# Kernel tuning notes

Hardware: AMD Instinct MI355X
Metric: run time of the kernel (lower is better)

The kernel has to match this reference:

```python
import jax, jax.numpy as jnp
import numpy as np

B, S, D = 2, 2048, 1024
H, E = 16, 64          # n_heads, head_dim
DFF = 4096             # intermediate
R_ATTN, R_OUT, R_FF = 32, 512, 512
LN_EPS = 1e-5
SCALE = 1.0 / np.sqrt(E)


def setup_inputs() -> dict:
    key = jax.random.key(0)
    ks = jax.random.split(key, 24)
    s = 0.02
    inp = {
        "hidden_states": jax.random.normal(ks[0], (B, S, D), jnp.float32),
        "ln1_w": jnp.ones((D,), jnp.float32),
        "ln1_b": jnp.zeros((D,), jnp.float32),
        "q_U": jax.random.normal(ks[1], (H, E, R_ATTN), jnp.float32) * s,
        "q_V": jax.random.normal(ks[2], (H, R_ATTN, D), jnp.float32) * s,
        "q_bias": jax.random.normal(ks[3], (H, E), jnp.float32) * s,
        "k_U": jax.random.normal(ks[4], (H, E, R_ATTN), jnp.float32) * s,
        "k_V": jax.random.normal(ks[5], (H, R_ATTN, D), jnp.float32) * s,
        "k_bias": jax.random.normal(ks[6], (H, E), jnp.float32) * s,
        "v_U": jax.random.normal(ks[7], (H, E, R_ATTN), jnp.float32) * s,
        "v_V": jax.random.normal(ks[8], (H, R_ATTN, D), jnp.float32) * s,
        "v_bias": jax.random.normal(ks[9], (H, E), jnp.float32) * s,
        "out_U": jax.random.normal(ks[10], (D, R_OUT), jnp.float32) * s,
        "out_V": jax.random.normal(ks[11], (R_OUT, D), jnp.float32) * s,
        "out_bias": jnp.zeros((D,), jnp.float32),
        "ln2_w": jnp.ones((D,), jnp.float32),
        "ln2_b": jnp.zeros((D,), jnp.float32),
        "fc1_U": jax.random.normal(ks[12], (DFF, R_FF), jnp.float32) * s,
        "fc1_V": jax.random.normal(ks[13], (R_FF, D), jnp.float32) * s,
        "fc1_bias": jnp.zeros((DFF,), jnp.float32),
        "fc2_U": jax.random.normal(ks[14], (D, R_FF), jnp.float32) * s,
        "fc2_V": jax.random.normal(ks[15], (R_FF, DFF), jnp.float32) * s,
        "fc2_bias": jnp.zeros((D,), jnp.float32),
    }
    return inp


def _layernorm(x, w, b):
    mu = jnp.mean(x, axis=-1, keepdims=True)
    var = jnp.mean(jnp.square(x - mu), axis=-1, keepdims=True)
    return (x - mu) * jax.lax.rsqrt(var + LN_EPS) * w + b


def _per_head_svd(x, U, V, bias):
    # x: [b,s,d]; V: [h,r,d]; U: [h,e,r]; bias: [h,e] -> [b,h,s,e]
    t = jnp.einsum("bsd,hrd->bhsr", x, V)
    return jnp.einsum("bhsr,her->bhse", t, U) + bias[None, :, None, :]


def reference(hidden_states, ln1_w, ln1_b, q_U, q_V, q_bias, k_U, k_V, k_bias,
              v_U, v_V, v_bias, out_U, out_V, out_bias, ln2_w, ln2_b,
              fc1_U, fc1_V, fc1_bias, fc2_U, fc2_V, fc2_bias):
    b, s, d = hidden_states.shape
    normed = _layernorm(hidden_states, ln1_w, ln1_b)

    q = _per_head_svd(normed, q_U, q_V, q_bias)  # [b,h,s,e]
    k = _per_head_svd(normed, k_U, k_V, k_bias)
    v = _per_head_svd(normed, v_U, v_V, v_bias)

    scores = jnp.einsum("bhqe,bhke->bhqk", q, k) * SCALE
    causal = jnp.tril(jnp.ones((s, s), dtype=bool))
    scores = jnp.where(causal, scores, -jnp.inf)
    probs = jax.nn.softmax(scores, axis=-1)
    attn = jnp.einsum("bhqk,bhke->bhqe", probs, v)
    attn = attn.transpose(0, 2, 1, 3).reshape(b, s, d)  # [b,s,d]

    attn = jnp.einsum("bsr,dr->bsd", jnp.einsum("bsd,rd->bsr", attn, out_V), out_U) + out_bias
    hidden_states = hidden_states + attn

    normed = _layernorm(hidden_states, ln2_w, ln2_b)
    ff = jnp.einsum("bsr,fr->bsf", jnp.einsum("bsd,rd->bsr", normed, fc1_V), fc1_U) + fc1_bias
    ff = jax.nn.gelu(ff, approximate=False)  # exact erf gelu as in torch F.gelu
    ff = jnp.einsum("bsr,dr->bsd", jnp.einsum("bsf,rf->bsr", ff, fc2_V), fc2_U) + fc2_bias
    hidden_states = hidden_states + ff
    return (hidden_states,)
```

## Files before the change

kernel.cpp:

```cpp
#include <hip/hip_runtime.h>
#include <hip/hip_bf16.h>
#include <math.h>

#define Bc 2
#define Sc 2048
#define Dc 1024
#define Hc 16
#define Ec 64
#define DFFc 4096
#define SCALEc 0.125f
#define SCLOG2E 0.18033688f
#define LN_EPSc 1e-5f
#define BH_STRIDE 131072

typedef short bf16x8 __attribute__((ext_vector_type(8)));
typedef unsigned short u16x4 __attribute__((ext_vector_type(4)));
typedef unsigned short u16x8 __attribute__((ext_vector_type(8)));
typedef float f32x4 __attribute__((ext_vector_type(4)));
typedef float f32x16 __attribute__((ext_vector_type(16)));
typedef unsigned int u32x4 __attribute__((ext_vector_type(4)));
#define MFMA16(a, b, c) __builtin_amdgcn_mfma_f32_16x16x32_bf16(a, b, c, 0, 0, 0)
#define MFMA32(a, b, c) __builtin_amdgcn_mfma_f32_32x32x16_bf16(a, b, c, 0, 0, 0)
#define GLDS16(g, l)                                                            \
  __builtin_amdgcn_global_load_lds((const __attribute__((address_space(1))) void*)(g), \
                                   (__attribute__((address_space(3))) void*)(l), 16, 0, 0)

static __device__ __forceinline__ unsigned short f2bf(float x) {
  unsigned u = __float_as_uint(x);
  unsigned r = (u + 0x7FFFu + ((u >> 16) & 1u)) >> 16;
  return (unsigned short)r;
}
static __device__ __forceinline__ unsigned cvtpk(float lo, float hi) {
  unsigned r;
  asm("v_cvt_pk_bf16_f32 %0, %1, %2" : "=v"(r) : "v"(lo), "v"(hi));
  return r;
}

__global__ __launch_bounds__(256) void convert9(
    const float* __restrict__ s0, const float* __restrict__ s1, const float* __restrict__ s2,
    const float* __restrict__ s3, const float* __restrict__ s4, const float* __restrict__ s5,
    const float* __restrict__ s6, const float* __restrict__ s7, const float* __restrict__ s8,
    unsigned short* __restrict__ wsu) {
  int i = (blockIdx.x * 256 + threadIdx.x) * 4;
  const float* s;
  int off;
  if (i < 3145728) {
    int seg = i >> 19;
    off = i & 524287;
    s = (seg == 0) ? s0 : (seg == 1) ? s1 : (seg == 2) ? s2
        : (seg == 3) ? s3 : (seg == 4) ? s4 : s5;
  } else if (i < 5242880) { s = s6; off = i - 3145728; }
  else if (i < 7340032)   { s = s7; off = i - 5242880; }
  else if (i < 7864320)   { s = s8; off = i - 7340032; }
  else return;
  float4 v = *(const float4*)(s + off);
  u16x4 o = {f2bf(v.x), f2bf(v.y), f2bf(v.z), f2bf(v.w)};
  *(u16x4*)(wsu + i) = o;
}

__global__ __launch_bounds__(256) void ln_bf16(const float* __restrict__ x,
                                               const float* __restrict__ w,
                                               const float* __restrict__ b,
                                               unsigned short* __restrict__ out) {
  __shared__ float sm[8];
  int row = blockIdx.x;
  int tid = threadIdx.x;
  const float* xr = x + (size_t)row * Dc;
  float v[4];
  float sum = 0.f;
#pragma unroll
  for (int i = 0; i < 4; ++i) { v[i] = xr[tid + i * 256]; sum += v[i]; }
#pragma unroll
  for (int off = 32; off > 0; off >>= 1) sum += __shfl_down(sum, off, 64);
  if ((tid & 63) == 0) sm[tid >> 6] = sum;
  __syncthreads();
  float mean = (sm[0] + sm[1] + sm[2] + sm[3]) * (1.f / Dc);
  float var = 0.f;
#pragma unroll
  for (int i = 0; i < 4; ++i) { float d0 = v[i] - mean; var += d0 * d0; }
#pragma unroll
  for (int off = 32; off > 0; off >>= 1) var += __shfl_down(var, off, 64);
  if ((tid & 63) == 0) sm[4 + (tid >> 6)] = var;
  __syncthreads();
  float rstd = rsqrtf((sm[4] + sm[5] + sm[6] + sm[7]) * (1.f / Dc) + LN_EPSc);
  unsigned short* orow = out + (size_t)row * Dc;
#pragma unroll
  for (int i = 0; i < 4; ++i) {
    int c = tid + i * 256;
    orow[c] = f2bf((v[i] - mean) * rstd * w[c] + b[c]);
  }
}

template <int BM, int BN>
__global__ __launch_bounds__(256) void gemm_bf16(const unsigned short* __restrict__ A,
                                                 const unsigned short* __restrict__ W,
                                                 float* __restrict__ Cf,
                                                 unsigned short* __restrict__ Cb,
                                                 const float* __restrict__ bias,
                                                 const float* __restrict__ res,
                                                 int M, int N, int K, int gelu) {
  constexpr int BK = 64;
  constexpr int MT = BM / 32;
  constexpr int NT = BN / 32;
  __shared__ unsigned short As[2][BM * BK];
  __shared__ unsigned short Bs[2][BN * BK];
  int tid = threadIdx.x;
  int lane = tid & 63;
  int wid = tid >> 6;
  int cl = lane & 15, grp = lane >> 4;
  int wr = wid >> 1, wc = wid & 1;
  const unsigned short* Ab = A + (size_t)(blockIdx.y * BM) * K;
  const unsigned short* Wb = W + (size_t)(blockIdx.x * BN) * K;
  f32x4 acc[MT][NT];
  f32x4 z4 = {0.f, 0.f, 0.f, 0.f};
#pragma unroll
  for (int i = 0; i < MT; ++i)
#pragma unroll
    for (int j = 0; j < NT; ++j) acc[i][j] = z4;
  int r0 = tid >> 3;
  int c0 = (tid & 7) * 8;

#define STAGE(buf, k0)                                                         \
  {                                                                            \
    _Pragma("unroll") for (int l = 0; l < BM / 32; ++l) {                      \
      int row = r0 + l * 32;                                                   \
      int sc = c0 ^ ((row & 7) * 8);                                           \
      GLDS16(Ab + (size_t)row * K + (k0) + sc, &As[buf][(tid + l * 256) * 8]); \
    }                                                                          \
    _Pragma("unroll") for (int l = 0; l < BN / 32; ++l) {                      \
      int row = r0 + l * 32;                                                   \
      int sc = c0 ^ ((row & 7) * 8);                                           \
      GLDS16(Wb + (size_t)row * K + (k0) + sc, &Bs[buf][(tid + l * 256) * 8]); \
    }                                                                          \
  }

  int nt = K / BK;
  STAGE(0, 0)
  __syncthreads();
  for (int t = 0; t < nt; ++t) {
    int cur = t & 1;
    if (t + 1 < nt) STAGE(cur ^ 1, (t + 1) * BK)
#pragma unroll
    for (int kk = 0; kk < 2; ++kk) {
      bf16x8 af[MT], bfr[NT];
#pragma unroll
      for (int i = 0; i < MT; ++i) {
        int row = wr * (BM / 2) + i * 16 + cl;
        af[i] = *(const bf16x8*)&As[cur][row * BK + ((kk * 32 + grp * 8) ^ ((row & 7) * 8))];
      }
#pragma unroll
      for (int j = 0; j < NT; ++j) {
        int row = wc * (BN / 2) + j * 16 + cl;
        bfr[j] = *(const bf16x8*)&Bs[cur][row * BK + ((kk * 32 + grp * 8) ^ ((row & 7) * 8))];
      }
#pragma unroll
      for (int i = 0; i < MT; ++i)
#pragma unroll
        for (int j = 0; j < NT; ++j) acc[i][j] = MFMA16(af[i], bfr[j], acc[i][j]);
    }
    __syncthreads();
  }
#undef STAGE

#pragma unroll
  for (int i = 0; i < MT; ++i) {
    int row = blockIdx.y * BM + wr * (BM / 2) + i * 16 + grp * 4;
#pragma unroll
    for (int j = 0; j < NT; ++j) {
      int col = blockIdx.x * BN + wc * (BN / 2) + j * 16 + cl;
      float bv = bias ? bias[col] : 0.f;
#pragma unroll
      for (int r = 0; r < 4; ++r) {
        float v = acc[i][j][r] + bv;
        if (gelu) v = 0.5f * v * (1.f + erff(v * 0.70710678118f));
        if (res) v += res[(size_t)(row + r) * N + col];
        if (Cb) Cb[(size_t)(row + r) * N + col] = f2bf(v);
        else Cf[(size_t)(row + r) * N + col] = v;
      }
    }
  }
}

__global__ __launch_bounds__(256) void expand_all(const float* __restrict__ t,
                                                  const float* __restrict__ qU,
                                                  const float* __restrict__ kU,
                                                  const float* __restrict__ vU,
                                                  const float* __restrict__ qB,
                                                  const float* __restrict__ kB,
                                                  const float* __restrict__ vB,
                                                  unsigned short* __restrict__ qO,
                                                  unsigned short* __restrict__ kO,
                                                  unsigned short* __restrict__ vO) {
  __shared__ float Us[64][33];
  __shared__ float Ts[32][33];
  int blk = blockIdx.x;
  int kind = blk >> 11;
  int inner = blk & 2047;
  int sb = inner & 63;
  int h = (inner >> 6) & 15;
  int b = inner >> 10;
  int bh = b * Hc + h;
  int tid = threadIdx.x;
  const float* U = (kind == 0) ? qU : (kind == 1) ? kU : vU;
  const float* bias = (kind == 0) ? qB : (kind == 1) ? kB : vB;
  int toff = kind * 512;
  for (int i = tid; i < 64 * 32; i += 256) Us[i >> 5][i & 31] = U[h * 2048 + i];
  for (int i = tid; i < 32 * 32; i += 256) {
    int sr = i >> 5, r = i & 31;
    Ts[sr][r] = t[(size_t)(b * Sc + sb * 32 + sr) * 1536 + toff + h * 32 + r];
  }
  __syncthreads();
  if (kind < 2) {
    unsigned short* out = (kind == 0) ? qO : kO;
    float prescale = (kind == 0) ? SCLOG2E : 1.0f;
    int s = tid >> 3;
    int ec = tid & 7;
    float acc[8];
#pragma unroll
    for (int j = 0; j < 8; ++j) acc[j] = bias[h * 64 + ec * 8 + j];
    for (int r = 0; r < 32; ++r) {
      float tv = Ts[s][r];
#pragma unroll
      for (int j = 0; j < 8; ++j) acc[j] += tv * Us[ec * 8 + j][r];
    }
    u16x8 v8;
#pragma unroll
    for (int j = 0; j < 8; ++j) v8[j] = f2bf(acc[j] * prescale);
    int es = ec >> 1, hi = ec & 1;
    int lane = s + hi * 32;
    *(u16x8*)(out + (size_t)bh * BH_STRIDE + (size_t)(((sb * 4 + es) * 64 + lane)) * 8) = v8;
  } else {
    int e = tid & 63;
    int sg = tid >> 6;
    float bv = bias[h * 64 + e];
    u16x8 v8;
#pragma unroll
    for (int si = 0; si < 8; ++si) {
      int sr = sg * 8 + si;
      float acc = bv;
#pragma unroll
      for (int r = 0; r < 32; ++r) acc += Ts[sr][r] * Us[e][r];
      v8[si] = f2bf(acc);
    }
    int eo = e >> 5, ll = e & 31;
    int h2 = sg >> 1, hi = sg & 1;
    int ix = eo * 2 + h2;
    int lane = ll + hi * 32;
    *(u16x8*)(vO + (size_t)bh * BH_STRIDE + (size_t)(((sb * 4 + ix) * 64 + lane)) * 8) = v8;
  }
}

__global__ __launch_bounds__(256) void attn_mfma(const unsigned short* __restrict__ qf_,
                                                 const unsigned short* __restrict__ kf_,
                                                 const unsigned short* __restrict__ vf_,
                                                 unsigned short* __restrict__ out) {
  __shared__ float MS[2][34][64];
  int tid = threadIdx.x;
  int wid = tid >> 6;
  int lane = tid & 63;
  int ll = lane & 31;
  int hi = lane >> 5;
  int blk = blockIdx.x;
  int qt = 63 - (blk >> 5);
  int bh = blk & 31;
  int b = bh >> 4, h = bh & 15;
  const unsigned short* qb = qf_ + (size_t)bh * BH_STRIDE;
  const unsigned short* kb = kf_ + (size_t)bh * BH_STRIDE;
  const unsigned short* vb = vf_ + (size_t)bh * BH_STRIDE;
  int q0 = qt * 32;
  int nt = qt + 1;
  int full = nt - 1;
  int fs = wid * full / 4;
  int fe = (wid + 1) * full / 4;

  bf16x8 qf[4];
#pragma unroll
  for (int es = 0; es < 4; ++es)
    qf[es] = *(const bf16x8*)(qb + (size_t)((qt * 4 + es) * 64 + lane) * 8);

  f32x16 accO[2] = {};
  float m = -1e30f, l = 0.f;

  int t = fs;
  for (; t + 1 < fe; t += 2) {
    bf16x8 ka[4], kb2[4];
#pragma unroll
    for (int es = 0; es < 4; ++es) {
      ka[es] = *(const bf16x8*)(kb + (size_t)((t * 4 + es) * 64 + lane) * 8);
      kb2[es] = *(const bf16x8*)(kb + (size_t)(((t + 1) * 4 + es) * 64 + lane) * 8);
    }
    f32x16 cA = {}, cB = {};
    __builtin_amdgcn_s_setprio(1);
    cA = MFMA32(ka[0], qf[0], cA);
    cA = MFMA32(ka[1], qf[1], cA);
    cA = MFMA32(ka[2], qf[2], cA);
    cA = MFMA32(ka[3], qf[3], cA);
    cB = MFMA32(kb2[0], qf[0], cB);
    cB = MFMA32(kb2[1], qf[1], cB);
    cB = MFMA32(kb2[2], qf[2], cB);
    cB = MFMA32(kb2[3], qf[3], cB);
    __builtin_amdgcn_s_setprio(0);
    float s[32];
#pragma unroll
    for (int r = 0; r < 16; ++r) { s[r] = cA[r]; s[16 + r] = cB[r]; }
    float mx[16];
#pragma unroll
    for (int r = 0; r < 16; ++r) mx[r] = fmaxf(s[r], s[16 + r]);
#pragma unroll
    for (int st = 8; st > 0; st >>= 1)
#pragma unroll
      for (int r = 0; r < 8; ++r)
        if (r < st) mx[r] = fmaxf(mx[r], mx[r + st]);
    float tmax = fmaxf(mx[0], __shfl_xor(mx[0], 32, 64));
    if (!__all(tmax <= m)) {
      float mn = fmaxf(m, tmax);
      float corr = exp2f(m - mn);
      m = mn;
      l *= corr;
#pragma unroll
      for (int r = 0; r < 16; ++r) { accO[0][r] *= corr; accO[1][r] *= corr; }
    }
#pragma unroll
    for (int r = 0; r < 32; ++r) s[r] = exp2f(s[r] - m);
#pragma unroll
    for (int r = 0; r < 16; ++r) mx[r] = s[r] + s[16 + r];
#pragma unroll
    for (int st = 8; st > 0; st >>= 1)
#pragma unroll
      for (int r = 0; r < 8; ++r)
        if (r < st) mx[r] += mx[r + st];
    l += mx[0];
    bf16x8 va[4], vb2[4];
#pragma unroll
    for (int ix = 0; ix < 4; ++ix) {
      va[ix] = *(const bf16x8*)(vb + (size_t)((t * 4 + ix) * 64 + lane) * 8);
      vb2[ix] = *(const bf16x8*)(vb + (size_t)(((t + 1) * 4 + ix) * 64 + lane) * 8);
    }
    unsigned wA0 = cvtpk(s[0], s[1]), wA1 = cvtpk(s[2], s[3]);
    unsigned wA2 = cvtpk(s[4], s[5]), wA3 = cvtpk(s[6], s[7]);
    unsigned wA4 = cvtpk(s[8], s[9]), wA5 = cvtpk(s[10], s[11]);
    unsigned wA6 = cvtpk(s[12], s[13]), wA7 = cvtpk(s[14], s[15]);
    unsigned wB0 = cvtpk(s[16], s[17]), wB1 = cvtpk(s[18], s[19]);
    unsigned wB2 = cvtpk(s[20], s[21]), wB3 = cvtpk(s[22], s[23]);
    unsigned wB4 = cvtpk(s[24], s[25]), wB5 = cvtpk(s[26], s[27]);
    unsigned wB6 = cvtpk(s[28], s[29]), wB7 = cvtpk(s[30], s[31]);
    asm("v_permlane32_swap_b32 %0, %1" : "+v"(wA0), "+v"(wA2));
    asm("v_permlane32_swap_b32 %0, %1" : "+v"(wA1), "+v"(wA3));
    asm("v_permlane32_swap_b32 %0, %1" : "+v"(wA4), "+v"(wA6));
    asm("v_permlane32_swap_b32 %0, %1" : "+v"(wA5), "+v"(wA7));
    asm("v_permlane32_swap_b32 %0, %1" : "+v"(wB0), "+v"(wB2));
    asm("v_permlane32_swap_b32 %0, %1" : "+v"(wB1), "+v"(wB3));
    asm("v_permlane32_swap_b32 %0, %1" : "+v"(wB4), "+v"(wB6));
    asm("v_permlane32_swap_b32 %0, %1" : "+v"(wB5), "+v"(wB7));
    u32x4 pA0 = {wA0, wA1, wA2, wA3}, pA1 = {wA4, wA5, wA6, wA7};
    u32x4 pB0 = {wB0, wB1, wB2, wB3}, pB1 = {wB4, wB5, wB6, wB7};
    bf16x8 bA0 = __builtin_bit_cast(bf16x8, pA0), bA1 = __builtin_bit_cast(bf16x8, pA1);
    bf16x8 bB0 = __builtin_bit_cast(bf16x8, pB0), bB1 = __builtin_bit_cast(bf16x8, pB1);
    __builtin_amdgcn_s_setprio(1);
    accO[0] = MFMA32(va[0], bA0, accO[0]);
    accO[0] = MFMA32(va[1], bA1, accO[0]);
    accO[0] = MFMA32(vb2[0], bB0, accO[0]);
    accO[0] = MFMA32(vb2[1], bB1, accO[0]);
    accO[1] = MFMA32(va[2], bA0, accO[1]);
    accO[1] = MFMA32(va[3], bA1, accO[1]);
    accO[1] = MFMA32(vb2[2], bB0, accO[1]);
    accO[1] = MFMA32(vb2[3], bB1, accO[1]);
    __builtin_amdgcn_s_setprio(0);
  }

#define ATT_ONE(T, MASKED)                                                          \
  {                                                                                 \
    bf16x8 kf1[4];                                                                  \
    _Pragma("unroll") for (int es = 0; es < 4; ++es)                                \
      kf1[es] = *(const bf16x8*)(kb + (size_t)(((T) * 4 + es) * 64 + lane) * 8);    \
    f32x16 c = {};                                                                  \
    __builtin_amdgcn_s_setprio(1);                                                  \
    c = MFMA32(kf1[0], qf[0], c);                                                   \
    c = MFMA32(kf1[1], qf[1], c);                                                   \
    c = MFMA32(kf1[2], qf[2], c);                                                   \
    c = MFMA32(kf1[3], qf[3], c);                                                   \
    __builtin_amdgcn_s_setprio(0);                                                  \
    float s1[16];                                                                   \
    _Pragma("unroll") for (int r = 0; r < 16; ++r) {                                \
      s1[r] = c[r];                                                                 \
      if (MASKED) {                                                                 \
        int keyloc = (r & 3) + 8 * (r >> 2) + 4 * hi;                               \
        if (keyloc > ll) s1[r] = -1e30f;                                            \
      }                                                                             \
    }                                                                               \
    float u0 = fmaxf(fmaxf(fmaxf(s1[0], s1[1]), fmaxf(s1[2], s1[3])),               \
                     fmaxf(fmaxf(s1[4], s1[5]), fmaxf(s1[6], s1[7])));              \
    float u1 = fmaxf(fmaxf(fmaxf(s1[8], s1[9]), fmaxf(s1[10], s1[11])),             \
                     fmaxf(fmaxf(s1[12], s1[13]), fmaxf(s1[14], s1[15])));          \
    float tmax = fmaxf(u0, u1);                                                     \
    tmax = fmaxf(tmax, __shfl_xor(tmax, 32, 64));                                   \
    if (!__all(tmax <= m)) {                                                        \
      float mn = fmaxf(m, tmax);                                                    \
      float corr = exp2f(m - mn);                                                   \
      m = mn;                                                                       \
      l *= corr;                                                                    \
      _Pragma("unroll") for (int r = 0; r < 16; ++r) {                              \
        accO[0][r] *= corr; accO[1][r] *= corr;                                     \
      }                                                                             \
    }                                                                               \
    float lp = 0.f;                                                                 \
    _Pragma("unroll") for (int r = 0; r < 16; ++r) { s1[r] = exp2f(s1[r] - m); lp += s1[r]; } \
    l += lp;                                                                        \
    bf16x8 vf1[4];                                                                  \
    _Pragma("unroll") for (int ix = 0; ix < 4; ++ix)                                \
      vf1[ix] = *(const bf16x8*)(vb + (size_t)(((T) * 4 + ix) * 64 + lane) * 8);    \
    unsigned w0 = cvtpk(s1[0], s1[1]), w1 = cvtpk(s1[2], s1[3]);                    \
    unsigned w2 = cvtpk(s1[4], s1[5]), w3 = cvtpk(s1[6], s1[7]);                    \
    unsigned w4 = cvtpk(s1[8], s1[9]), w5 = cvtpk(s1[10], s1[11]);                  \
    unsigned w6 = cvtpk(s1[12], s1[13]), w7 = cvtpk(s1[14], s1[15]);                \
    asm("v_permlane32_swap_b32 %0, %1" : "+v"(w0), "+v"(w2));                       \
    asm("v_permlane32_swap_b32 %0, %1" : "+v"(w1), "+v"(w3));                       \
    asm("v_permlane32_swap_b32 %0, %1" : "+v"(w4), "+v"(w6));                       \
    asm("v_permlane32_swap_b32 %0, %1" : "+v"(w5), "+v"(w7));                       \
    u32x4 pw0 = {w0, w1, w2, w3};                                                   \
    u32x4 pw1 = {w4, w5, w6, w7};                                                   \
    bf16x8 pb0 = __builtin_bit_cast(bf16x8, pw0);                                   \
    bf16x8 pb1 = __builtin_bit_cast(bf16x8, pw1);                                   \
    __builtin_amdgcn_s_setprio(1);                                                  \
    accO[0] = MFMA32(vf1[0], pb0, accO[0]);                                         \
    accO[0] = MFMA32(vf1[1], pb1, accO[0]);                                         \
    accO[1] = MFMA32(vf1[2], pb0, accO[1]);                                         \
    accO[1] = MFMA32(vf1[3], pb1, accO[1]);                                         \
    __builtin_amdgcn_s_setprio(0);                                                  \
  }

  if (t < fe) ATT_ONE(t, false)
  if (wid == 3) ATT_ONE(full, true)
#undef ATT_ONE

  auto publish = [&](int slot) {
#pragma unroll
    for (int r = 0; r < 16; ++r) {
      MS[slot][r][lane] = accO[0][r];
      MS[slot][16 + r][lane] = accO[1][r];
    }
    MS[slot][32][lane] = m;
    MS[slot][33][lane] = l;
  };
  auto merge = [&](int slot) {
    float mw = MS[slot][32][lane];
    float lw = MS[slot][33][lane];
    float ms = fmaxf(m, mw);
    float sc = exp2f(m - ms);
    float sw = exp2f(mw - ms);
    m = ms;
    l = l * sc + lw * sw;
#pragma unroll
    for (int r = 0; r < 16; ++r) {
      accO[0][r] = accO[0][r] * sc + MS[slot][r][lane] * sw;
      accO[1][r] = accO[1][r] * sc + MS[slot][16 + r][lane] * sw;
    }
  };
  if (wid == 1) publish(0);
  if (wid == 3) publish(1);
  __syncthreads();
  if (wid == 0) merge(0);
  if (wid == 2) merge(1);
  __syncthreads();
  if (wid == 2) publish(0);
  __syncthreads();
  if (wid == 0) {
    merge(0);
    float ltot = l + __shfl_xor(l, 32, 64);
    float inv = 1.f / ltot;
    unsigned short* orow = out + (size_t)(b * Sc + q0 + ll) * Dc + h * Ec;
#pragma unroll
    for (int eo = 0; eo < 2; ++eo)
#pragma unroll
      for (int r = 0; r < 16; ++r) {
        int e = eo * 32 + (r & 3) + 8 * (r >> 2) + 4 * hi;
        orow[e] = f2bf(accO[eo][r] * inv);
      }
  }
}

extern "C" void kernel_launch(void* const* d_in, const int* in_sizes, int n_in,
                              void* d_out, int out_size, void* d_ws, size_t ws_size,
                              hipStream_t stream) {
  const float* hidden = (const float*)d_in[0];
  const float* ln1_w = (const float*)d_in[1];
  const float* ln1_b = (const float*)d_in[2];
  const float* q_U = (const float*)d_in[3];
  const float* q_V = (const float*)d_in[4];
  const float* q_bias = (const float*)d_in[5];
  const float* k_U = (const float*)d_in[6];
  const float* k_V = (const float*)d_in[7];
  const float* k_bias = (const float*)d_in[8];
  const float* v_U = (const float*)d_in[9];
  const float* v_V = (const float*)d_in[10];
  const float* v_bias = (const float*)d_in[11];
  const float* out_U = (const float*)d_in[12];
  const float* out_V = (const float*)d_in[13];
  const float* out_bias = (const float*)d_in[14];
  const float* ln2_w = (const float*)d_in[15];
  const float* ln2_b = (const float*)d_in[16];
  const float* fc1_U = (const float*)d_in[17];
  const float* fc1_V = (const float*)d_in[18];
  const float* fc1_bias = (const float*)d_in[19];
  const float* fc2_U = (const float*)d_in[20];
  const float* fc2_V = (const float*)d_in[21];
  const float* fc2_bias = (const float*)d_in[22];
  float* out = (float*)d_out;
  float* ws = (float*)d_ws;
  unsigned short* wsu = (unsigned short*)d_ws;

  unsigned short* wQKV = wsu;
  unsigned short* wOUTV = wsu + 1572864;
  unsigned short* wOUTU = wsu + 2097152;
  unsigned short* wFC1V = wsu + 2621440;
  unsigned short* wFC1U = wsu + 3145728;
  unsigned short* wFC2V = wsu + 5242880;
  unsigned short* wFC2U = wsu + 7340032;

  float* h1 = ws + 4194304;
  unsigned short* attn_out = (unsigned short*)(ws + 6291456);
  unsigned short* normed = (unsigned short*)(ws + 8388608);
  float* rb = ws + 10485760;
  unsigned short* rbB = (unsigned short*)(ws + 10485760);
  unsigned short* ff = (unsigned short*)(ws + 11534336);
  unsigned short* qbuf = (unsigned short*)(ws + 16777216);
  unsigned short* kbuf = (unsigned short*)(ws + 18874368);
  unsigned short* rbG = (unsigned short*)(ws + 19922944);
  unsigned short* vtbuf = (unsigned short*)(ws + 20971520);

  const int M = Bc * Sc;
  dim3 blk(256);

  convert9<<<7680, blk, 0, stream>>>(q_V, k_V, v_V, out_V, out_U, fc1_V, fc1_U, fc2_V, fc2_U, wsu);

  ln_bf16<<<M, blk, 0, stream>>>(hidden, ln1_w, ln1_b, normed);

  gemm_bf16<64, 64><<<dim3(24, 64), blk, 0, stream>>>(normed, wQKV, rb, nullptr, nullptr, nullptr,
                                                      M, 1536, Dc, 0);
  expand_all<<<6144, blk, 0, stream>>>(rb, q_U, k_U, v_U, q_bias, k_bias, v_bias,
                                       qbuf, kbuf, vtbuf);

  attn_mfma<<<2048, blk, 0, stream>>>(qbuf, kbuf, vtbuf, attn_out);

  gemm_bf16<64, 64><<<dim3(8, 64), blk, 0, stream>>>(attn_out, wOUTV, nullptr, rbB, nullptr, nullptr,
                                                     M, 512, Dc, 0);
  gemm_bf16<64, 64><<<dim3(16, 64), blk, 0, stream>>>(rbB, wOUTU, h1, nullptr, out_bias, hidden,
                                                      M, Dc, 512, 0);

  ln_bf16<<<M, blk, 0, stream>>>(h1, ln2_w, ln2_b, normed);
  gemm_bf16<64, 64><<<dim3(8, 64), blk, 0, stream>>>(normed, wFC1V, nullptr, rbB, nullptr, nullptr,
                                                     M, 512, Dc, 0);
  gemm_bf16<128, 64><<<dim3(64, 32), blk, 0, stream>>>(rbB, wFC1U, nullptr, ff, fc1_bias, nullptr,
                                                       M, DFFc, 512, 1);
  gemm_bf16<64, 64><<<dim3(8, 64), blk, 0, stream>>>(ff, wFC2V, nullptr, rbG, nullptr, nullptr,
                                                     M, 512, DFFc, 0);
  gemm_bf16<64, 64><<<dim3(16, 64), blk, 0, stream>>>(rbG, wFC2U, out, nullptr, fc2_bias, h1,
                                                      M, Dc, 512, 0);
}
```

Before: 281.4 us.

## Restructure attention to share LDS-staged K/V tiles across four query waves

The attention kernel changes from one 32-query tile per block (split-K across four waves with an LDS merge) to a 128-query tile per block where each wave owns 32 queries. K/V tiles of 64 keys are staged into double-buffered LDS with async global-to-LDS loads and shared by all four waves, which removes the cross-wave softmax merge and cuts redundant global K/V reads. The grid shrinks from 2048 to 512 blocks with a heavy/light ordering for causal balance. In exchange there is a barrier per tile, waves idle on tiles past their diagonal, and fewer blocks give less parallelism.

```diff
diff --git a/kernel.cpp b/kernel.cpp
--- a/kernel.cpp
+++ b/kernel.cpp
@@ -254,229 +254,156 @@
                                                  const unsigned short* __restrict__ kf_,
                                                  const unsigned short* __restrict__ vf_,
                                                  unsigned short* __restrict__ out) {
-  __shared__ float MS[2][34][64];
+  __shared__ unsigned short Ks[2][4096];
+  __shared__ unsigned short Vs[2][4096];
   int tid = threadIdx.x;
   int wid = tid >> 6;
   int lane = tid & 63;
   int ll = lane & 31;
   int hi = lane >> 5;
-  int blk = blockIdx.x;
-  int qt = 63 - (blk >> 5);
-  int bh = blk & 31;
+  int bid = blockIdx.x;
+  int bh = bid & 31;
+  int qb = (bid < 256) ? (15 - (bid >> 5)) : ((bid - 256) >> 5);
   int b = bh >> 4, h = bh & 15;
-  const unsigned short* qb = qf_ + (size_t)bh * BH_STRIDE;
-  const unsigned short* kb = kf_ + (size_t)bh * BH_STRIDE;
-  const unsigned short* vb = vf_ + (size_t)bh * BH_STRIDE;
-  int q0 = qt * 32;
-  int nt = qt + 1;
-  int full = nt - 1;
-  int fs = wid * full / 4;
-  int fe = (wid + 1) * full / 4;
+  const unsigned short* qbp = qf_ + (size_t)bh * BH_STRIDE;
+  const unsigned short* kbp = kf_ + (size_t)bh * BH_STRIDE;
+  const unsigned short* vbp = vf_ + (size_t)bh * BH_STRIDE;
+  int d = qb * 4 + wid;
+  int q0w = qb * 128 + wid * 32;
+  int NT = qb * 2 + 2;
 
   bf16x8 qf[4];
 #pragma unroll
   for (int es = 0; es < 4; ++es)
-    qf[es] = *(const bf16x8*)(qb + (size_t)((qt * 4 + es) * 64 + lane) * 8);
+    qf[es] = *(const bf16x8*)(qbp + (size_t)d * 2048 + es * 512 + lane * 8);
 
   f32x16 accO[2] = {};
   float m = -1e30f, l = 0.f;
 
-  int t = fs;
-  for (; t + 1 < fe; t += 2) {
-    bf16x8 ka[4], kb2[4];
-#pragma unroll
-    for (int es = 0; es < 4; ++es) {
-      ka[es] = *(const bf16x8*)(kb + (size_t)((t * 4 + es) * 64 + lane) * 8);
-      kb2[es] = *(const bf16x8*)(kb + (size_t)(((t + 1) * 4 + es) * 64 + lane) * 8);
-    }
-    f32x16 cA = {}, cB = {};
-    __builtin_amdgcn_s_setprio(1);
-    cA = MFMA32(ka[0], qf[0], cA);
-    cA = MFMA32(ka[1], qf[1], cA);
-    cA = MFMA32(ka[2], qf[2], cA);
-    cA = MFMA32(ka[3], qf[3], cA);
-    cB = MFMA32(kb2[0], qf[0], cB);
-    cB = MFMA32(kb2[1], qf[1], cB);
-    cB = MFMA32(kb2[2], qf[2], cB);
-    cB = MFMA32(kb2[3], qf[3], cB);
-    __builtin_amdgcn_s_setprio(0);
-    float s[32];
-#pragma unroll
-    for (int r = 0; r < 16; ++r) { s[r] = cA[r]; s[16 + r] = cB[r]; }
-    float mx[16];
-#pragma unroll
-    for (int r = 0; r < 16; ++r) mx[r] = fmaxf(s[r], s[16 + r]);
-#pragma unroll
-    for (int st = 8; st > 0; st >>= 1)
-#pragma unroll
-      for (int r = 0; r < 8; ++r)
-        if (r < st) mx[r] = fmaxf(mx[r], mx[r + st]);
-    float tmax = fmaxf(mx[0], __shfl_xor(mx[0], 32, 64));
-    if (!__all(tmax <= m)) {
-      float mn = fmaxf(m, tmax);
-      float corr = exp2f(m - mn);
-      m = mn;
-      l *= corr;
-#pragma unroll
-      for (int r = 0; r < 16; ++r) { accO[0][r] *= corr; accO[1][r] *= corr; }
-    }
-#pragma unroll
-    for (int r = 0; r < 32; ++r) s[r] = exp2f(s[r] - m);
-#pragma unroll
-    for (int r = 0; r < 16; ++r) mx[r] = s[r] + s[16 + r];
-#pragma unroll
-    for (int st = 8; st > 0; st >>= 1)
-#pragma unroll
-      for (int r = 0; r < 8; ++r)
-        if (r < st) mx[r] += mx[r + st];
-    l += mx[0];
-    bf16x8 va[4], vb2[4];
-#pragma unroll
-    for (int ix = 0; ix < 4; ++ix) {
-      va[ix] = *(const bf16x8*)(vb + (size_t)((t * 4 + ix) * 64 + lane) * 8);
-      vb2[ix] = *(const bf16x8*)(vb + (size_t)(((t + 1) * 4 + ix) * 64 + lane) * 8);
-    }
-    unsigned wA0 = cvtpk(s[0], s[1]), wA1 = cvtpk(s[2], s[3]);
-    unsigned wA2 = cvtpk(s[4], s[5]), wA3 = cvtpk(s[6], s[7]);
-    unsigned wA4 = cvtpk(s[8], s[9]), wA5 = cvtpk(s[10], s[11]);
-    unsigned wA6 = cvtpk(s[12], s[13]), wA7 = cvtpk(s[14], s[15]);
-    unsigned wB0 = cvtpk(s[16], s[17]), wB1 = cvtpk(s[18], s[19]);
-    unsigned wB2 = cvtpk(s[20], s[21]), wB3 = cvtpk(s[22], s[23]);
-    unsigned wB4 = cvtpk(s[24], s[25]), wB5 = cvtpk(s[26], s[27]);
-    unsigned wB6 = cvtpk(s[28], s[29]), wB7 = cvtpk(s[30], s[31]);
-    asm("v_permlane32_swap_b32 %0, %1" : "+v"(wA0), "+v"(wA2));
-    asm("v_permlane32_swap_b32 %0, %1" : "+v"(wA1), "+v"(wA3));
-    asm("v_permlane32_swap_b32 %0, %1" : "+v"(wA4), "+v"(wA6));
-    asm("v_permlane32_swap_b32 %0, %1" : "+v"(wA5), "+v"(wA7));
-    asm("v_permlane32_swap_b32 %0, %1" : "+v"(wB0), "+v"(wB2));
-    asm("v_permlane32_swap_b32 %0, %1" : "+v"(wB1), "+v"(wB3));
-    asm("v_permlane32_swap_b32 %0, %1" : "+v"(wB4), "+v"(wB6));
-    asm("v_permlane32_swap_b32 %0, %1" : "+v"(wB5), "+v"(wB7));
-    u32x4 pA0 = {wA0, wA1, wA2, wA3}, pA1 = {wA4, wA5, wA6, wA7};
-    u32x4 pB0 = {wB0, wB1, wB2, wB3}, pB1 = {wB4, wB5, wB6, wB7};
-    bf16x8 bA0 = __builtin_bit_cast(bf16x8, pA0), bA1 = __builtin_bit_cast(bf16x8, pA1);
-    bf16x8 bB0 = __builtin_bit_cast(bf16x8, pB0), bB1 = __builtin_bit_cast(bf16x8, pB1);
-    __builtin_amdgcn_s_setprio(1);
-    accO[0] = MFMA32(va[0], bA0, accO[0]);
-    accO[0] = MFMA32(va[1], bA1, accO[0]);
-    accO[0] = MFMA32(vb2[0], bB0, accO[0]);
-    accO[0] = MFMA32(vb2[1], bB1, accO[0]);
-    accO[1] = MFMA32(va[2], bA0, accO[1]);
-    accO[1] = MFMA32(va[3], bA1, accO[1]);
-    accO[1] = MFMA32(vb2[2], bB0, accO[1]);
-    accO[1] = MFMA32(vb2[3], bB1, accO[1]);
-    __builtin_amdgcn_s_setprio(0);
-  }
-
-#define ATT_ONE(T, MASKED)                                                          \
-  {                                                                                 \
-    bf16x8 kf1[4];                                                                  \
-    _Pragma("unroll") for (int es = 0; es < 4; ++es)                                \
-      kf1[es] = *(const bf16x8*)(kb + (size_t)(((T) * 4 + es) * 64 + lane) * 8);    \
-    f32x16 c = {};                                                                  \
-    __builtin_amdgcn_s_setprio(1);                                                  \
-    c = MFMA32(kf1[0], qf[0], c);                                                   \
-    c = MFMA32(kf1[1], qf[1], c);                                                   \
-    c = MFMA32(kf1[2], qf[2], c);                                                   \
-    c = MFMA32(kf1[3], qf[3], c);                                                   \
-    __builtin_amdgcn_s_setprio(0);                                                  \
-    float s1[16];                                                                   \
-    _Pragma("unroll") for (int r = 0; r < 16; ++r) {                                \
-      s1[r] = c[r];                                                                 \
-      if (MASKED) {                                                                 \
-        int keyloc = (r & 3) + 8 * (r >> 2) + 4 * hi;                               \
-        if (keyloc > ll) s1[r] = -1e30f;                                            \
-      }                                                                             \
-    }                                                                               \
-    float u0 = fmaxf(fmaxf(fmaxf(s1[0], s1[1]), fmaxf(s1[2], s1[3])),               \
-                     fmaxf(fmaxf(s1[4], s1[5]), fmaxf(s1[6], s1[7])));              \
-    float u1 = fmaxf(fmaxf(fmaxf(s1[8], s1[9]), fmaxf(s1[10], s1[11])),             \
-                     fmaxf(fmaxf(s1[12], s1[13]), fmaxf(s1[14], s1[15])));          \
-    float tmax = fmaxf(u0, u1);                                                     \
-    tmax = fmaxf(tmax, __shfl_xor(tmax, 32, 64));                                   \
-    if (!__all(tmax <= m)) {                                                        \
-      float mn = fmaxf(m, tmax);                                                    \
-      float corr = exp2f(m - mn);                                                   \
-      m = mn;                                                                       \
-      l *= corr;                                                                    \
-      _Pragma("unroll") for (int r = 0; r < 16; ++r) {                              \
-        accO[0][r] *= corr; accO[1][r] *= corr;                                     \
-      }                                                                             \
-    }                                                                               \
-    float lp = 0.f;                                                                 \
-    _Pragma("unroll") for (int r = 0; r < 16; ++r) { s1[r] = exp2f(s1[r] - m); lp += s1[r]; } \
-    l += lp;                                                                        \
-    bf16x8 vf1[4];                                                                  \
-    _Pragma("unroll") for (int ix = 0; ix < 4; ++ix)                                \
-      vf1[ix] = *(const bf16x8*)(vb + (size_t)(((T) * 4 + ix) * 64 + lane) * 8);    \
-    unsigned w0 = cvtpk(s1[0], s1[1]), w1 = cvtpk(s1[2], s1[3]);                    \
-    unsigned w2 = cvtpk(s1[4], s1[5]), w3 = cvtpk(s1[6], s1[7]);                    \
-    unsigned w4 = cvtpk(s1[8], s1[9]), w5 = cvtpk(s1[10], s1[11]);                  \
-    unsigned w6 = cvtpk(s1[12], s1[13]), w7 = cvtpk(s1[14], s1[15]);                \
-    asm("v_permlane32_swap_b32 %0, %1" : "+v"(w0), "+v"(w2));                       \
-    asm("v_permlane32_swap_b32 %0, %1" : "+v"(w1), "+v"(w3));                       \
-    asm("v_permlane32_swap_b32 %0, %1" : "+v"(w4), "+v"(w6));                       \
-    asm("v_permlane32_swap_b32 %0, %1" : "+v"(w5), "+v"(w7));                       \
-    u32x4 pw0 = {w0, w1, w2, w3};                                                   \
-    u32x4 pw1 = {w4, w5, w6, w7};                                                   \
-    bf16x8 pb0 = __builtin_bit_cast(bf16x8, pw0);                                   \
-    bf16x8 pb1 = __builtin_bit_cast(bf16x8, pw1);                                   \
-    __builtin_amdgcn_s_setprio(1);                                                  \
-    accO[0] = MFMA32(vf1[0], pb0, accO[0]);                                         \
-    accO[0] = MFMA32(vf1[1], pb1, accO[0]);                                         \
-    accO[1] = MFMA32(vf1[2], pb0, accO[1]);                                         \
-    accO[1] = MFMA32(vf1[3], pb1, accO[1]);                                         \
-    __builtin_amdgcn_s_setprio(0);                                                  \
-  }
-
-  if (t < fe) ATT_ONE(t, false)
-  if (wid == 3) ATT_ONE(full, true)
-#undef ATT_ONE
-
-  auto publish = [&](int slot) {
+  GLDS16(kbp + tid * 8, &Ks[0][tid * 8]);
+  GLDS16(kbp + 2048 + tid * 8, &Ks[0][2048 + tid * 8]);
+  GLDS16(vbp + tid * 8, &Vs[0][tid * 8]);
+  GLDS16(vbp + 2048 + tid * 8, &Vs[0][2048 + tid * 8]);
+  __syncthreads();
+
+  for (int pt = 0; pt < NT; ++pt) {
+    int buf = pt & 1;
+    if (pt + 1 < NT) {
+      const unsigned short* kg = kbp + (size_t)(pt + 1) * 4096;
+      const unsigned short* vg = vbp + (size_t)(pt + 1) * 4096;
+      GLDS16(kg + tid * 8, &Ks[buf ^ 1][tid * 8]);
+      GLDS16(kg + 2048 + tid * 8, &Ks[buf ^ 1][2048 + tid * 8]);
+      GLDS16(vg + tid * 8, &Vs[buf ^ 1][tid * 8]);
+      GLDS16(vg + 2048 + tid * 8, &Vs[buf ^ 1][2048 + tid * 8]);
+    }
+    int kt0 = pt * 2;
+    if (kt0 <= d) {
+      bool mA = (kt0 == d);
+      bool mBf = (kt0 + 1 > d);
+      bool mBd = (kt0 + 1 == d);
+      bf16x8 ka[4], kb2[4];
+#pragma unroll
+      for (int es = 0; es < 4; ++es) {
+        ka[es] = *(const bf16x8*)&Ks[buf][es * 512 + lane * 8];
+        kb2[es] = *(const bf16x8*)&Ks[buf][2048 + es * 512 + lane * 8];
+      }
+      f32x16 cA = {}, cB = {};
+      __builtin_amdgcn_s_setprio(1);
+      cA = MFMA32(ka[0], qf[0], cA);
+      cA = MFMA32(ka[1], qf[1], cA);
+      cA = MFMA32(ka[2], qf[2], cA);
+      cA = MFMA32(ka[3], qf[3], cA);
+      cB = MFMA32(kb2[0], qf[0], cB);
+      cB = MFMA32(kb2[1], qf[1], cB);
+      cB = MFMA32(kb2[2], qf[2], cB);
+      cB = MFMA32(kb2[3], qf[3], cB);
+      __builtin_amdgcn_s_setprio(0);
+      float s[32];
+#pragma unroll
+      for (int r = 0; r < 16; ++r) {
+        int keyloc = (r & 3) + 8 * (r >> 2) + 4 * hi;
+        s[r] = cA[r];
+        if (mA && keyloc > ll) s[r] = -1e30f;
+        s[16 + r] = cB[r];
+        if (mBf || (mBd && keyloc > ll)) s[16 + r] = -1e30f;
+      }
+      float mx[16];
+#pragma unroll
+      for (int r = 0; r < 16; ++r) mx[r] = fmaxf(s[r], s[16 + r]);
+#pragma unroll
+      for (int st = 8; st > 0; st >>= 1)
+#pragma unroll
+        for (int r = 0; r < 8; ++r)
+          if (r < st) mx[r] = fmaxf(mx[r], mx[r + st]);
+      float tmax = fmaxf(mx[0], __shfl_xor(mx[0], 32, 64));
+      if (!__all(tmax <= m)) {
+        float mn = fmaxf(m, tmax);
+        float corr = exp2f(m - mn);
+        m = mn;
+        l *= corr;
+#pragma unroll
+        for (int r = 0; r < 16; ++r) { accO[0][r] *= corr; accO[1][r] *= corr; }
+      }
+#pragma unroll
+      for (int r = 0; r < 32; ++r) s[r] = exp2f(s[r] - m);
+#pragma unroll
+      for (int r = 0; r < 16; ++r) mx[r] = s[r] + s[16 + r];
+#pragma unroll
+      for (int st = 8; st > 0; st >>= 1)
+#pragma unroll
+        for (int r = 0; r < 8; ++r)
+          if (r < st) mx[r] += mx[r + st];
+      l += mx[0];
+      bf16x8 va[4], vb2[4];
+#pragma unroll
+      for (int ix = 0; ix < 4; ++ix) {
+        va[ix] = *(const bf16x8*)&Vs[buf][ix * 512 + lane * 8];
+        vb2[ix] = *(const bf16x8*)&Vs[buf][2048 + ix * 512 + lane * 8];
+      }
+      unsigned wA0 = cvtpk(s[0], s[1]), wA1 = cvtpk(s[2], s[3]);
+      unsigned wA2 = cvtpk(s[4], s[5]), wA3 = cvtpk(s[6], s[7]);
+      unsigned wA4 = cvtpk(s[8], s[9]), wA5 = cvtpk(s[10], s[11]);
+      unsigned wA6 = cvtpk(s[12], s[13]), wA7 = cvtpk(s[14], s[15]);
+      unsigned wB0 = cvtpk(s[16], s[17]), wB1 = cvtpk(s[18], s[19]);
+      unsigned wB2 = cvtpk(s[20], s[21]), wB3 = cvtpk(s[22], s[23]);
+      unsigned wB4 = cvtpk(s[24], s[25]), wB5 = cvtpk(s[26], s[27]);
+      unsigned wB6 = cvtpk(s[28], s[29]), wB7 = cvtpk(s[30], s[31]);
+      asm("v_permlane32_swap_b32 %0, %1" : "+v"(wA0), "+v"(wA2));
+      asm("v_permlane32_swap_b32 %0, %1" : "+v"(wA1), "+v"(wA3));
+      asm("v_permlane32_swap_b32 %0, %1" : "+v"(wA4), "+v"(wA6));
+      asm("v_permlane32_swap_b32 %0, %1" : "+v"(wA5), "+v"(wA7));
+      asm("v_permlane32_swap_b32 %0, %1" : "+v"(wB0), "+v"(wB2));
+      asm("v_permlane32_swap_b32 %0, %1" : "+v"(wB1), "+v"(wB3));
+      asm("v_permlane32_swap_b32 %0, %1" : "+v"(wB4), "+v"(wB6));
+      asm("v_permlane32_swap_b32 %0, %1" : "+v"(wB5), "+v"(wB7));
+      u32x4 pA0 = {wA0, wA1, wA2, wA3}, pA1 = {wA4, wA5, wA6, wA7};
+      u32x4 pB0 = {wB0, wB1, wB2, wB3}, pB1 = {wB4, wB5, wB6, wB7};
+      bf16x8 bA0 = __builtin_bit_cast(bf16x8, pA0), bA1 = __builtin_bit_cast(bf16x8, pA1);
+      bf16x8 bB0 = __builtin_bit_cast(bf16x8, pB0), bB1 = __builtin_bit_cast(bf16x8, pB1);
+      __builtin_amdgcn_s_setprio(1);
+      accO[0] = MFMA32(va[0], bA0, accO[0]);
+      accO[0] = MFMA32(va[1], bA1, accO[0]);
+      accO[0] = MFMA32(vb2[0], bB0, accO[0]);
+      accO[0] = MFMA32(vb2[1], bB1, accO[0]);
+      accO[1] = MFMA32(va[2], bA0, accO[1]);
+      accO[1] = MFMA32(va[3], bA1, accO[1]);
+      accO[1] = MFMA32(vb2[2], bB0, accO[1]);
+      accO[1] = MFMA32(vb2[3], bB1, accO[1]);
+      __builtin_amdgcn_s_setprio(0);
+    }
+    __syncthreads();
+  }
+
+  float ltot = l + __shfl_xor(l, 32, 64);
+  float inv = 1.f / ltot;
+  unsigned short* orow = out + (size_t)(b * Sc + q0w + ll) * Dc + h * Ec;
+#pragma unroll
+  for (int eo = 0; eo < 2; ++eo)
 #pragma unroll
     for (int r = 0; r < 16; ++r) {
-      MS[slot][r][lane] = accO[0][r];
-      MS[slot][16 + r][lane] = accO[1][r];
-    }
-    MS[slot][32][lane] = m;
-    MS[slot][33][lane] = l;
-  };
-  auto merge = [&](int slot) {
-    float mw = MS[slot][32][lane];
-    float lw = MS[slot][33][lane];
-    float ms = fmaxf(m, mw);
-    float sc = exp2f(m - ms);
-    float sw = exp2f(mw - ms);
-    m = ms;
-    l = l * sc + lw * sw;
-#pragma unroll
-    for (int r = 0; r < 16; ++r) {
-      accO[0][r] = accO[0][r] * sc + MS[slot][r][lane] * sw;
-      accO[1][r] = accO[1][r] * sc + MS[slot][16 + r][lane] * sw;
-    }
-  };
-  if (wid == 1) publish(0);
-  if (wid == 3) publish(1);
-  __syncthreads();
-  if (wid == 0) merge(0);
-  if (wid == 2) merge(1);
-  __syncthreads();
-  if (wid == 2) publish(0);
-  __syncthreads();
-  if (wid == 0) {
-    merge(0);
-    float ltot = l + __shfl_xor(l, 32, 64);
-    float inv = 1.f / ltot;
-    unsigned short* orow = out + (size_t)(b * Sc + q0 + ll) * Dc + h * Ec;
-#pragma unroll
-    for (int eo = 0; eo < 2; ++eo)
-#pragma unroll
-      for (int r = 0; r < 16; ++r) {
-        int e = eo * 32 + (r & 3) + 8 * (r >> 2) + 4 * hi;
-        orow[e] = f2bf(accO[eo][r] * inv);
-      }
-  }
+      int e = eo * 32 + (r & 3) + 8 * (r >> 2) + 4 * hi;
+      orow[e] = f2bf(accO[eo][r] * inv);
+    }
 }
 
 extern "C" void kernel_launch(void* const* d_in, const int* in_sizes, int n_in,
@@ -540,7 +467,7 @@
   expand_all<<<6144, blk, 0, stream>>>(rb, q_U, k_U, v_U, q_bias, k_bias, v_bias,
                                        qbuf, kbuf, vtbuf);
 
-  attn_mfma<<<2048, blk, 0, stream>>>(qbuf, kbuf, vtbuf, attn_out);
+  attn_mfma<<<512, blk, 0, stream>>>(qbuf, kbuf, vtbuf, attn_out);
 
   gemm_bf16<64, 64><<<dim3(8, 64), blk, 0, stream>>>(attn_out, wOUTV, nullptr, rbB, nullptr, nullptr,
                                                      M, 512, Dc, 0);
```

New measurement: 298.2 us. 6.0% more time.
